# Kernel tuning notes

Measured on AMD Instinct MI355X. Metric: run time of the kernel, lower is better.

Reference implementation:

```python
import jax, jax.numpy as jnp
import numpy as np

T = 0.04
PIC_NUM = 4  # images per identity (hardcoded in SP_loss)


def setup_inputs() -> dict:
    key = jax.random.key(0)
    N, D = 8192, 256  # 2048 identities x 4 images, 256-dim ReID features
    x = jax.random.normal(key, (N, D), dtype=jnp.float32)
    x = x / jnp.linalg.norm(x, axis=1, keepdims=True)  # L2-normalize (cosine sims)
    return {"x": x}


def reference(x):
    N = x.shape[0]
    G = N // PIC_NUM  # number of identity groups
    s = (x @ x.T) / T  # [N, N] scaled similarity matrix

    # Diagonal 4x4 blocks: within-class similarities. [G, 4, 4]
    d4 = s.reshape(G, PIC_NUM, G, PIC_NUM)
    gidx = jnp.arange(G)
    pos = d4[gidx, :, gidx, :]  # [G, 4, 4]

    # hard positive: -T * log( sum_{i,j in class} exp(-dot_ij / T) )  (soft-min)
    hard_pos = -T * jax.nn.logsumexp(-pos.reshape(G, PIC_NUM * PIC_NUM), axis=1)

    # least-hard positive: T * log( sum_i 1 / (sum_j exp(-dot_ij / T)) )
    lse_row = jax.nn.logsumexp(-pos, axis=2)           # [G, 4] = log sum_j exp(-dot/T)
    least_pos = T * jax.nn.logsumexp(-lse_row, axis=1)  # [G]

    # negatives: T * log( sum_{i in class, j not in class} exp(dot_ij / T) )
    col_group = jnp.arange(N) // PIC_NUM              # [N]
    same = col_group[None, :] == gidx[:, None]        # [G, N] same-class column mask
    s3 = s.reshape(G, PIC_NUM, N)
    neg_masked = jnp.where(same[:, None, :], -jnp.inf, s3)
    neg = T * jax.nn.logsumexp(neg_masked.reshape(G, PIC_NUM * N), axis=1)  # [G]

    # Original detaches all three S vectors before forming the loss.
    hard_pos = jax.lax.stop_gradient(hard_pos)
    least_pos = jax.lax.stop_gradient(least_pos)
    neg = jax.lax.stop_gradient(neg)

    # alpha: harmonic mean of (hard, least-hard) when hard >= 0, else 0
    alpha = jnp.where(hard_pos >= 0.0,
                      2.0 * least_pos * hard_pos / (hard_pos + least_pos),
                      0.0)
    margin = alpha * hard_pos + (1.0 - alpha) * least_pos
    # log(1 + exp(z)) == softplus(z), numerically stable, same math
    loss = jnp.mean(jax.nn.softplus((neg - margin) / T))
    return loss
```

## Files before the change

### kernel.cpp

```cpp
#include <hip/hip_runtime.h>
#include <hip/hip_bf16.h>
#include <math.h>


#define NROWS 8192
#define DDIM  256
#define NGRP  2048
#define NTB   64
#define T_CONST 0.04f
#define INV_T   25.0f

typedef __attribute__((ext_vector_type(8))) short bf16x8_t;
typedef __attribute__((ext_vector_type(4))) float f32x4_t;

typedef const __attribute__((address_space(1))) void gv_t;
typedef __attribute__((address_space(3))) void lv_t;

__device__ __forceinline__ unsigned short f2bf_rne(float f) {
    unsigned int u = __float_as_uint(f);
    unsigned int r = 0x7fffu + ((u >> 16) & 1u);
    return (unsigned short)((u + r) >> 16);
}

__device__ __forceinline__ void gll16(const unsigned short* g, unsigned short* l) {
    __builtin_amdgcn_global_load_lds((gv_t*)g, (lv_t*)l, 16, 0, 0);
}

__global__ __launch_bounds__(256) void prep_kernel(const float* __restrict__ x,
                                                   unsigned short* __restrict__ xb,
                                                   float* __restrict__ rowsum,
                                                   float* __restrict__ margin) {
    const int b = blockIdx.x;
    if (b < 2048) {
        int gid = b * 256 + threadIdx.x;
        int i = gid * 4;
        float4 v = *(const float4*)(x + i);
        ushort4 o;
        o.x = f2bf_rne(v.x); o.y = f2bf_rne(v.y); o.z = f2bf_rne(v.z); o.w = f2bf_rne(v.w);
        *(ushort4*)(xb + i) = o;
        if (gid < NROWS) rowsum[gid] = 0.f;
        return;
    }
    const int g = (b - 2048) * 4 + (threadIdx.x >> 6);
    const int lane = threadIdx.x & 63;
    const float* xr = x + (size_t)g * 4 * DDIM;
    float a[16];
#pragma unroll
    for (int k = 0; k < 16; ++k) a[k] = 0.f;
    for (int e = lane; e < DDIM; e += 64) {
        float vv[4];
        vv[0] = xr[e];
        vv[1] = xr[DDIM + e];
        vv[2] = xr[2 * DDIM + e];
        vv[3] = xr[3 * DDIM + e];
#pragma unroll
        for (int i = 0; i < 4; ++i)
#pragma unroll
            for (int j = 0; j < 4; ++j)
                a[i * 4 + j] = fmaf(vv[i], vv[j], a[i * 4 + j]);
    }
#pragma unroll
    for (int k = 0; k < 16; ++k) {
        float t = a[k];
        t += __shfl_xor(t, 32, 64);
        t += __shfl_xor(t, 16, 64);
        t += __shfl_xor(t, 8, 64);
        t += __shfl_xor(t, 4, 64);
        t += __shfl_xor(t, 2, 64);
        t += __shfl_xor(t, 1, 64);
        a[k] = t;
    }
    if (lane == 0) {
        float pos[16];
#pragma unroll
        for (int k = 0; k < 16; ++k) pos[k] = a[k] * INV_T;

        float mx = -pos[0];
#pragma unroll
        for (int k = 1; k < 16; ++k) mx = fmaxf(mx, -pos[k]);
        float se = 0.f;
#pragma unroll
        for (int k = 0; k < 16; ++k) se += __expf(-pos[k] - mx);
        float hard_pos = -T_CONST * (mx + __logf(se));

        float lse_row[4];
#pragma unroll
        for (int i = 0; i < 4; ++i) {
            float m2 = -pos[i * 4];
#pragma unroll
            for (int j = 1; j < 4; ++j) m2 = fmaxf(m2, -pos[i * 4 + j]);
            float s2 = 0.f;
#pragma unroll
            for (int j = 0; j < 4; ++j) s2 += __expf(-pos[i * 4 + j] - m2);
            lse_row[i] = m2 + __logf(s2);
        }
        float m3 = -lse_row[0];
#pragma unroll
        for (int i = 1; i < 4; ++i) m3 = fmaxf(m3, -lse_row[i]);
        float s3 = 0.f;
#pragma unroll
        for (int i = 0; i < 4; ++i) s3 += __expf(-lse_row[i] - m3);
        float least_pos = T_CONST * (m3 + __logf(s3));

        float alpha = (hard_pos >= 0.f)
                          ? (2.f * least_pos * hard_pos) / (hard_pos + least_pos)
                          : 0.f;
        margin[g] = alpha * hard_pos + (1.f - alpha) * least_pos;
    }
}

__global__ __launch_bounds__(256) void gemm_exp_rowsum(const unsigned short* __restrict__ xb,
                                                       float* __restrict__ rowsum) {
    __shared__ unsigned short Als[128 * 32];
    __shared__ unsigned short Bls[128 * 32];
    __shared__ float rowacc[128];
    __shared__ float colacc[128];

    const int idx = blockIdx.x;
    int bi = (int)((129.0f - sqrtf(16641.0f - 8.0f * (float)idx)) * 0.5f);
    while (bi * (129 - bi) / 2 > idx) --bi;
    while ((bi + 1) * (128 - bi) / 2 <= idx) ++bi;
    const int bj = bi + (idx - bi * (129 - bi) / 2);
    const int row0 = bi * 128;
    const int col0 = bj * 128;
    const bool diag = (bi == bj);

    const int tid = threadIdx.x;
    const int lane = tid & 63;
    const int w = tid >> 6;
    const int wrow = (w >> 1) * 64;
    const int wcol = (w & 1) * 64;
    const int quad = lane >> 4;
    const int l16 = lane & 15;
    const int swz = (l16 >> 1) & 3;
    const int srow = tid >> 2;
    const int kc = (tid & 3) ^ ((tid >> 3) & 3);

    if (tid < 128) { rowacc[tid] = 0.f; colacc[tid] = 0.f; }

    f32x4_t acc[4][4];
#pragma unroll
    for (int i = 0; i < 4; ++i)
#pragma unroll
        for (int j = 0; j < 4; ++j)
            acc[i][j] = (f32x4_t){0.f, 0.f, 0.f, 0.f};

    const unsigned short* ga = xb + (size_t)(row0 + srow) * DDIM + kc * 8;
    const unsigned short* gb = xb + (size_t)(col0 + srow) * DDIM + kc * 8;

    for (int kb = 0; kb < DDIM; kb += 32) {
        if (kb) __syncthreads();
        gll16(ga + kb,             &Als[tid * 8]);
        gll16(ga + kb + 64 * DDIM, &Als[2048 + tid * 8]);
        gll16(gb + kb,             &Bls[tid * 8]);
        gll16(gb + kb + 64 * DDIM, &Bls[2048 + tid * 8]);
        __syncthreads();

        bf16x8_t aF[4], bF[4];
#pragma unroll
        for (int mi = 0; mi < 4; ++mi)
            aF[mi] = *(const bf16x8_t*)&Als[(wrow + mi * 16 + l16) * 32 + (quad ^ swz) * 8];
#pragma unroll
        for (int ni = 0; ni < 4; ++ni)
            bF[ni] = *(const bf16x8_t*)&Bls[(wcol + ni * 16 + l16) * 32 + (quad ^ swz) * 8];
#pragma unroll
        for (int mi = 0; mi < 4; ++mi)
#pragma unroll
            for (int ni = 0; ni < 4; ++ni)
                acc[mi][ni] = __builtin_amdgcn_mfma_f32_16x16x32_bf16(aF[mi], bF[ni],
                                                                      acc[mi][ni], 0, 0, 0);
    }

    if (!diag) {
        float colv[4] = {0.f, 0.f, 0.f, 0.f};
#pragma unroll
        for (int mi = 0; mi < 4; ++mi) {
#pragma unroll
            for (int reg = 0; reg < 4; ++reg) {
                const int lrow = wrow + mi * 16 + quad * 4 + reg;
                float rv = 0.f;
#pragma unroll
                for (int ni = 0; ni < 4; ++ni) {
                    float e = __expf(acc[mi][ni][reg] * INV_T);
                    rv += e;
                    colv[ni] += e;
                }
                rv += __shfl_xor(rv, 1, 64);
                rv += __shfl_xor(rv, 2, 64);
                rv += __shfl_xor(rv, 4, 64);
                rv += __shfl_xor(rv, 8, 64);
                if (l16 == 0) atomicAdd(&rowacc[lrow], rv);
            }
        }
#pragma unroll
        for (int ni = 0; ni < 4; ++ni) {
            float cv = colv[ni];
            cv += __shfl_xor(cv, 16, 64);
            cv += __shfl_xor(cv, 32, 64);
            if (quad == 0) atomicAdd(&colacc[wcol + ni * 16 + l16], cv);
        }
    } else {
#pragma unroll
        for (int mi = 0; mi < 4; ++mi) {
#pragma unroll
            for (int reg = 0; reg < 4; ++reg) {
                const int lrow = wrow + mi * 16 + quad * 4 + reg;
                const int grp = (row0 + lrow) >> 2;
                float rv = 0.f;
#pragma unroll
                for (int ni = 0; ni < 4; ++ni) {
                    const int gcol = col0 + wcol + ni * 16 + l16;
                    rv += ((gcol >> 2) == grp) ? 0.f : __expf(acc[mi][ni][reg] * INV_T);
                }
                rv += __shfl_xor(rv, 1, 64);
                rv += __shfl_xor(rv, 2, 64);
                rv += __shfl_xor(rv, 4, 64);
                rv += __shfl_xor(rv, 8, 64);
                if (l16 == 0) atomicAdd(&rowacc[lrow], rv);
            }
        }
    }
    __syncthreads();
    if (tid < 128) {
        atomicAdd(&rowsum[row0 + tid], rowacc[tid]);
        if (!diag) atomicAdd(&rowsum[col0 + tid], colacc[tid]);
    }
}

__global__ __launch_bounds__(256) void finalize_kernel(const float* __restrict__ rowsum,
                                                       const float* __restrict__ margin,
                                                       float* __restrict__ out) {
    const int tid = threadIdx.x;
    float local = 0.f;
    for (int g = tid; g < NGRP; g += 256) {
        float s = rowsum[4 * g] + rowsum[4 * g + 1] + rowsum[4 * g + 2] + rowsum[4 * g + 3];
        float z = __logf(s) - margin[g] * INV_T;
        float sp = (z > 30.f) ? z : log1pf(__expf(z));
        local += sp;
    }
    local += __shfl_xor(local, 1, 64);
    local += __shfl_xor(local, 2, 64);
    local += __shfl_xor(local, 4, 64);
    local += __shfl_xor(local, 8, 64);
    local += __shfl_xor(local, 16, 64);
    local += __shfl_xor(local, 32, 64);
    __shared__ float wsum[4];
    if ((tid & 63) == 0) wsum[tid >> 6] = local;
    __syncthreads();
    if (tid == 0) out[0] = (wsum[0] + wsum[1] + wsum[2] + wsum[3]) * (1.f / (float)NGRP);
}

extern "C" void kernel_launch(void* const* d_in, const int* in_sizes, int n_in,
                              void* d_out, int out_size, void* d_ws, size_t ws_size,
                              hipStream_t stream) {
    const float* x = (const float*)d_in[0];
    float* out = (float*)d_out;

    unsigned short* xb = (unsigned short*)d_ws;
    float* rowsum = (float*)((char*)d_ws + (size_t)NROWS * DDIM * 2);
    float* margin = rowsum + NROWS;

    prep_kernel<<<2048 + 512, 256, 0, stream>>>(x, xb, rowsum, margin);
    gemm_exp_rowsum<<<NTB * (NTB + 1) / 2, 256, 0, stream>>>(xb, rowsum);
    finalize_kernel<<<1, 256, 0, stream>>>(rowsum, margin, out);
}
```

Baseline: 116.5 us.

## Double-buffer GEMM tiles, fuse finalize via last-block counter, use exp2

Adds double-buffered LDS staging so the next K-slice loads while the current one feeds the MFMAs. It removes the separate finalize launch: a global atomic counter, reset in prep, marks the last tile block, which then computes the loss. It also switches __expf to exp2f with a folded scale. The gains are less pipeline stall and one fewer launch, at the cost of more shared memory per block and a threadfence plus counter atomic in every block.

```diff
diff --git a/kernel.cpp b/kernel.cpp
--- a/kernel.cpp
+++ b/kernel.cpp
@@ -7,8 +7,10 @@
 #define DDIM  256
 #define NGRP  2048
 #define NTB   64
+#define NTILES (NTB * (NTB + 1) / 2)
 #define T_CONST 0.04f
 #define INV_T   25.0f
+#define EXP2_SCALE 36.06737602222409f
 
 typedef __attribute__((ext_vector_type(8))) short bf16x8_t;
 typedef __attribute__((ext_vector_type(4))) float f32x4_t;
@@ -29,7 +31,8 @@
 __global__ __launch_bounds__(256) void prep_kernel(const float* __restrict__ x,
                                                    unsigned short* __restrict__ xb,
                                                    float* __restrict__ rowsum,
-                                                   float* __restrict__ margin) {
+                                                   float* __restrict__ margin,
+                                                   unsigned int* __restrict__ counter) {
     const int b = blockIdx.x;
     if (b < 2048) {
         int gid = b * 256 + threadIdx.x;
@@ -39,6 +42,7 @@
         o.x = f2bf_rne(v.x); o.y = f2bf_rne(v.y); o.z = f2bf_rne(v.z); o.w = f2bf_rne(v.w);
         *(ushort4*)(xb + i) = o;
         if (gid < NROWS) rowsum[gid] = 0.f;
+        if (gid == 0) *counter = 0u;
         return;
     }
     const int g = (b - 2048) * 4 + (threadIdx.x >> 6);
@@ -110,11 +114,15 @@
 }
 
 __global__ __launch_bounds__(256) void gemm_exp_rowsum(const unsigned short* __restrict__ xb,
-                                                       float* __restrict__ rowsum) {
-    __shared__ unsigned short Als[128 * 32];
-    __shared__ unsigned short Bls[128 * 32];
+                                                       float* __restrict__ rowsum,
+                                                       const float* __restrict__ margin,
+                                                       unsigned int* __restrict__ counter,
+                                                       float* __restrict__ out) {
+    __shared__ unsigned short Als[2][128 * 32];
+    __shared__ unsigned short Bls[2][128 * 32];
     __shared__ float rowacc[128];
     __shared__ float colacc[128];
+    __shared__ unsigned int lastFlag;
 
     const int idx = blockIdx.x;
     int bi = (int)((129.0f - sqrtf(16641.0f - 8.0f * (float)idx)) * 0.5f);
@@ -148,21 +156,28 @@
     const unsigned short* ga = xb + (size_t)(row0 + srow) * DDIM + kc * 8;
     const unsigned short* gb = xb + (size_t)(col0 + srow) * DDIM + kc * 8;
 
-    for (int kb = 0; kb < DDIM; kb += 32) {
-        if (kb) __syncthreads();
-        gll16(ga + kb,             &Als[tid * 8]);
-        gll16(ga + kb + 64 * DDIM, &Als[2048 + tid * 8]);
-        gll16(gb + kb,             &Bls[tid * 8]);
-        gll16(gb + kb + 64 * DDIM, &Bls[2048 + tid * 8]);
+    gll16(ga,             &Als[0][tid * 8]);
+    gll16(ga + 64 * DDIM, &Als[0][2048 + tid * 8]);
+    gll16(gb,             &Bls[0][tid * 8]);
+    gll16(gb + 64 * DDIM, &Bls[0][2048 + tid * 8]);
+
+    for (int kb = 0; kb < 8; ++kb) {
+        const int cur = kb & 1;
         __syncthreads();
-
+        if (kb < 7) {
+            const int ko = (kb + 1) * 32;
+            gll16(ga + ko,             &Als[cur ^ 1][tid * 8]);
+            gll16(ga + ko + 64 * DDIM, &Als[cur ^ 1][2048 + tid * 8]);
+            gll16(gb + ko,             &Bls[cur ^ 1][tid * 8]);
+            gll16(gb + ko + 64 * DDIM, &Bls[cur ^ 1][2048 + tid * 8]);
+        }
         bf16x8_t aF[4], bF[4];
 #pragma unroll
         for (int mi = 0; mi < 4; ++mi)
-            aF[mi] = *(const bf16x8_t*)&Als[(wrow + mi * 16 + l16) * 32 + (quad ^ swz) * 8];
+            aF[mi] = *(const bf16x8_t*)&Als[cur][(wrow + mi * 16 + l16) * 32 + (quad ^ swz) * 8];
 #pragma unroll
         for (int ni = 0; ni < 4; ++ni)
-            bF[ni] = *(const bf16x8_t*)&Bls[(wcol + ni * 16 + l16) * 32 + (quad ^ swz) * 8];
+            bF[ni] = *(const bf16x8_t*)&Bls[cur][(wcol + ni * 16 + l16) * 32 + (quad ^ swz) * 8];
 #pragma unroll
         for (int mi = 0; mi < 4; ++mi)
 #pragma unroll
@@ -181,7 +196,7 @@
                 float rv = 0.f;
 #pragma unroll
                 for (int ni = 0; ni < 4; ++ni) {
-                    float e = __expf(acc[mi][ni][reg] * INV_T);
+                    float e = exp2f(acc[mi][ni][reg] * EXP2_SCALE);
                     rv += e;
                     colv[ni] += e;
                 }
@@ -210,7 +225,7 @@
 #pragma unroll
                 for (int ni = 0; ni < 4; ++ni) {
                     const int gcol = col0 + wcol + ni * 16 + l16;
-                    rv += ((gcol >> 2) == grp) ? 0.f : __expf(acc[mi][ni][reg] * INV_T);
+                    rv += ((gcol >> 2) == grp) ? 0.f : exp2f(acc[mi][ni][reg] * EXP2_SCALE);
                 }
                 rv += __shfl_xor(rv, 1, 64);
                 rv += __shfl_xor(rv, 2, 64);
@@ -225,29 +240,38 @@
         atomicAdd(&rowsum[row0 + tid], rowacc[tid]);
         if (!diag) atomicAdd(&rowsum[col0 + tid], colacc[tid]);
     }
-}
-
-__global__ __launch_bounds__(256) void finalize_kernel(const float* __restrict__ rowsum,
-                                                       const float* __restrict__ margin,
-                                                       float* __restrict__ out) {
-    const int tid = threadIdx.x;
-    float local = 0.f;
-    for (int g = tid; g < NGRP; g += 256) {
-        float s = rowsum[4 * g] + rowsum[4 * g + 1] + rowsum[4 * g + 2] + rowsum[4 * g + 3];
-        float z = __logf(s) - margin[g] * INV_T;
-        float sp = (z > 30.f) ? z : log1pf(__expf(z));
-        local += sp;
-    }
-    local += __shfl_xor(local, 1, 64);
-    local += __shfl_xor(local, 2, 64);
-    local += __shfl_xor(local, 4, 64);
-    local += __shfl_xor(local, 8, 64);
-    local += __shfl_xor(local, 16, 64);
-    local += __shfl_xor(local, 32, 64);
-    __shared__ float wsum[4];
-    if ((tid & 63) == 0) wsum[tid >> 6] = local;
+
+    __threadfence();
     __syncthreads();
-    if (tid == 0) out[0] = (wsum[0] + wsum[1] + wsum[2] + wsum[3]) * (1.f / (float)NGRP);
+    if (tid == 0) {
+        unsigned int prev = __hip_atomic_fetch_add(counter, 1u, __ATOMIC_ACQ_REL,
+                                                   __HIP_MEMORY_SCOPE_AGENT);
+        lastFlag = (prev == (unsigned int)(NTILES - 1)) ? 1u : 0u;
+    }
+    __syncthreads();
+    if (lastFlag) {
+        float local = 0.f;
+        for (int g = tid; g < NGRP; g += 256) {
+            float s = 0.f;
+#pragma unroll
+            for (int r = 0; r < 4; ++r)
+                s += __hip_atomic_load(&rowsum[4 * g + r], __ATOMIC_RELAXED,
+                                       __HIP_MEMORY_SCOPE_AGENT);
+            float z = __logf(s) - margin[g] * INV_T;
+            float sp = (z > 30.f) ? z : log1pf(__expf(z));
+            local += sp;
+        }
+        local += __shfl_xor(local, 1, 64);
+        local += __shfl_xor(local, 2, 64);
+        local += __shfl_xor(local, 4, 64);
+        local += __shfl_xor(local, 8, 64);
+        local += __shfl_xor(local, 16, 64);
+        local += __shfl_xor(local, 32, 64);
+        __shared__ float wsum[4];
+        if ((tid & 63) == 0) wsum[tid >> 6] = local;
+        __syncthreads();
+        if (tid == 0) out[0] = (wsum[0] + wsum[1] + wsum[2] + wsum[3]) * (1.f / (float)NGRP);
+    }
 }
 
 extern "C" void kernel_launch(void* const* d_in, const int* in_sizes, int n_in,
@@ -259,8 +283,8 @@
     unsigned short* xb = (unsigned short*)d_ws;
     float* rowsum = (float*)((char*)d_ws + (size_t)NROWS * DDIM * 2);
     float* margin = rowsum + NROWS;
-
-    prep_kernel<<<2048 + 512, 256, 0, stream>>>(x, xb, rowsum, margin);
-    gemm_exp_rowsum<<<NTB * (NTB + 1) / 2, 256, 0, stream>>>(xb, rowsum);
-    finalize_kernel<<<1, 256, 0, stream>>>(rowsum, margin, out);
-}
+    unsigned int* counter = (unsigned int*)(margin + NGRP);
+
+    prep_kernel<<<2048 + 512, 256, 0, stream>>>(x, xb, rowsum, margin, counter);
+    gemm_exp_rowsum<<<NTILES, 256, 0, stream>>>(xb, rowsum, margin, counter, out);
+}
```

After: 264.3 us. 127% more time.
